# Kernel tuning notes

Measured on AMD Instinct MI355X. Metric: run time of the kernel, lower is better.

## Reference

```python
import jax, jax.numpy as jnp
import numpy as np

HID, E, S, L_CAP, EPS = 768, 1536, 128, 512, 1e-5


def _rope_seq(x):
    """RoPE along axis 1. x: [b, n, 2, s]."""
    n, s = x.shape[1], x.shape[-1]
    half = s // 2
    inv_freq = jnp.power(10000.0, -jnp.arange(half, dtype=x.dtype) / half)  # [half]
    sinusoid = jnp.arange(n, dtype=x.dtype)[:, None, None] * inv_freq       # [n,1,half]
    sin, cos = jnp.sin(sinusoid), jnp.cos(sinusoid)
    x1, x2 = jnp.split(x, 2, axis=-1)
    return jnp.concatenate([x1 * cos - x2 * sin, x2 * cos + x1 * sin], axis=-1)


def setup_inputs() -> dict:
    key = jax.random.key(0)
    ks = jax.random.split(key, 6)
    B, L = 32, 512
    return {
        "x": jax.random.normal(ks[0], (B, L, HID), dtype=jnp.float32),
        "ln_gamma": jnp.ones((HID,), jnp.float32),
        "ln_beta": jnp.zeros((HID,), jnp.float32),
        "uv_W": jax.random.normal(ks[1], (HID, 2 * E + S), jnp.float32) * 0.02,
        "uv_b": jnp.zeros((2 * E + S,), jnp.float32),
        "gamma_qk": jax.random.normal(ks[2], (2, S), jnp.float32) * 0.02,
        "beta_qk": jnp.zeros((2, S), jnp.float32),
        "w_rel": jax.random.normal(ks[3], (2 * L_CAP - 1,), jnp.float32) * 0.02,
        "o_W": jax.random.normal(ks[4], (E, HID), jnp.float32) * 0.02,
        "o_b": jnp.zeros((HID,), jnp.float32),
    }


def reference(x, ln_gamma, ln_beta, uv_W, uv_b, gamma_qk, beta_qk, w_rel, o_W, o_b):
    L = x.shape[1]
    shortcut = x
    # LayerNorm
    mu = jnp.mean(x, axis=-1, keepdims=True)
    var = jnp.mean(jnp.square(x - mu), axis=-1, keepdims=True)
    xn = (x - mu) * jax.lax.rsqrt(var + EPS) * ln_gamma + ln_beta
    # uv projection + silu, split into u, v, base
    uv = jax.nn.silu(xn @ uv_W + uv_b)                       # [b, n, 2e+s]
    u, v, base = jnp.split(uv, [E, 2 * E], axis=-1)          # [b,n,e], [b,n,e], [b,n,s]
    # per-head affine then RoPE -> q, k
    base = base[..., None, :] * gamma_qk + beta_qk           # [b, n, 2, s]
    base = _rope_seq(base)
    q, k = base[..., 0, :], base[..., 1, :]
    # relu^2 attention kernel with Toeplitz relative position bias
    qk = jnp.einsum('bnd,bmd->bnm', q, k)
    idx = jnp.arange(L)
    bias = w_rel[idx[None, :] - idx[:, None] + L - 1]        # bias[i,j] = w[j-i+L-1]
    kernel = jnp.square(jax.nn.relu(qk / L + bias))
    # gated value aggregation + output projection + residual
    out = u * jnp.einsum('bnm,bme->bne', kernel, v)
    out = out @ o_W + o_b
    return out + shortcut
```

## Files before the change

### kernel.cpp

```cpp
#include <hip/hip_runtime.h>
#include <hip/hip_bf16.h>
#include <math.h>

typedef __bf16 bf16x8 __attribute__((ext_vector_type(8)));
typedef float f32x4 __attribute__((ext_vector_type(4)));
typedef unsigned short u16x4 __attribute__((ext_vector_type(4)));

#define AS1P const __attribute__((address_space(1))) void*
#define AS3P __attribute__((address_space(3))) void*

__device__ __forceinline__ float b2f(unsigned short h) {
    unsigned int u = ((unsigned int)h) << 16;
    return __builtin_bit_cast(float, u);
}
__device__ __forceinline__ unsigned short f2b(float f) {
    unsigned int u = __builtin_bit_cast(unsigned int, f);
    u += 0x7FFFu + ((u >> 16) & 1u);
    return (unsigned short)(u >> 16);
}
__device__ __forceinline__ float silu(float c) {
    return c * __builtin_amdgcn_rcpf(1.0f + __expf(-c));
}

__global__ __launch_bounds__(256) void k_convT(const float* __restrict__ src,
                                               unsigned short* __restrict__ dst,
                                               int R, int C) {
    __shared__ float tile[32][33];
    int tx = threadIdx.x, ty = threadIdx.y;
    int r0 = blockIdx.y << 5, c0 = blockIdx.x << 5;
#pragma unroll
    for (int i = 0; i < 4; ++i)
        tile[ty + 8 * i][tx] = src[(long long)(r0 + ty + 8 * i) * C + c0 + tx];
    __syncthreads();
#pragma unroll
    for (int i = 0; i < 4; ++i)
        dst[(long long)(c0 + ty + 8 * i) * R + r0 + tx] = f2b(tile[tx][ty + 8 * i]);
}

__global__ __launch_bounds__(256) void k_ln(const float* __restrict__ x,
                                            const float* __restrict__ g,
                                            const float* __restrict__ b,
                                            unsigned short* __restrict__ xn) {
    int row = blockIdx.x;
    int t = threadIdx.x;
    const float* xr = x + (long long)row * 768;
    float v0 = xr[t], v1 = xr[t + 256], v2 = xr[t + 512];
    float s = v0 + v1 + v2;
    float q = v0 * v0 + v1 * v1 + v2 * v2;
#pragma unroll
    for (int off = 32; off > 0; off >>= 1) {
        s += __shfl_xor(s, off);
        q += __shfl_xor(q, off);
    }
    __shared__ float ss[4], sq[4];
    int w = t >> 6;
    if ((t & 63) == 0) { ss[w] = s; sq[w] = q; }
    __syncthreads();
    float S_ = ss[0] + ss[1] + ss[2] + ss[3];
    float Q_ = sq[0] + sq[1] + sq[2] + sq[3];
    float mu = S_ * (1.0f / 768.0f);
    float var = Q_ * (1.0f / 768.0f) - mu * mu;
    float rs = rsqrtf(var + 1e-5f);
    unsigned short* xo = xn + (long long)row * 768;
    xo[t]       = f2b((v0 - mu) * rs * g[t]       + b[t]);
    xo[t + 256] = f2b((v1 - mu) * rs * g[t + 256] + b[t + 256]);
    xo[t + 512] = f2b((v2 - mu) * rs * g[t + 512] + b[t + 512]);
}

__global__ __launch_bounds__(128) void k_rope(const unsigned short* __restrict__ bS,
                                              const float* __restrict__ gqk,
                                              const float* __restrict__ bqk,
                                              unsigned short* __restrict__ q,
                                              unsigned short* __restrict__ k) {
    int row = blockIdx.x;
    int l = row & 511;
    int s = threadIdx.x;
    int j = s & 63;
    int partner = s ^ 64;
    float b0 = b2f(bS[(long long)row * 128 + s]);
    float bp = b2f(bS[(long long)row * 128 + partner]);
    float invf = __expf((float)j * -0.14391156831f);
    float th = (float)l * invf;
    float sn, cs;
    __sincosf(th, &sn, &cs);
    float sign = (s < 64) ? -1.0f : 1.0f;
    float preq  = b0 * gqk[s]           + bqk[s];
    float preqp = bp * gqk[partner]     + bqk[partner];
    q[(long long)row * 128 + s] = f2b(preq * cs + sign * preqp * sn);
    float prek  = b0 * gqk[128 + s]       + bqk[128 + s];
    float prekp = bp * gqk[128 + partner] + bqk[128 + partner];
    k[(long long)row * 128 + s] = f2b(prek * cs + sign * prekp * sn);
}

__global__ __launch_bounds__(256) void k_qk(const unsigned short* __restrict__ A,
                                            const unsigned short* __restrict__ B,
                                            const float* __restrict__ wrel,
                                            unsigned short* __restrict__ P) {
    __shared__ __align__(16) unsigned short As[128 * 64];
    __shared__ __align__(16) unsigned short Bs[128 * 64];
    int t = threadIdx.x;
    int w = t >> 6, lane = t & 63;
    int wr = w >> 1, wc = w & 1;
    int bx = blockIdx.x, by = blockIdx.y, bz = blockIdx.z;
    {
        int gx = gridDim.x, gy = gridDim.y;
        int nb = gx * gy * gridDim.z;
        int bid = (bz * gy + by) * gx + bx;
        int s = (bid & 7) * (nb >> 3) + (bid >> 3);
        bx = s % gx;
        by = (s / gx) % gy;
        bz = s / (gx * gy);
    }
    const unsigned short* Ab = A + (long long)bz * 512 * 128 + (long long)by * 128 * 128;
    const unsigned short* Bb = B + (long long)bz * 512 * 128 + (long long)bx * 128 * 128;

    f32x4 acc[4][4];
#pragma unroll
    for (int m = 0; m < 4; ++m)
#pragma unroll
        for (int n = 0; n < 4; ++n) acc[m][n] = (f32x4){0.f, 0.f, 0.f, 0.f};

    int rowA = (w << 3) + (lane >> 3);
    int colA = (lane & 7) << 3;

    for (int k0 = 0; k0 < 128; k0 += 64) {
#pragma unroll
        for (int i = 0; i < 4; ++i) {
            int r = (i << 5) + rowA;
            __builtin_amdgcn_global_load_lds(
                (AS1P)(Ab + (long long)r * 128 + k0 + colA),
                (AS3P)(&As[(i << 11) + (w << 9)]), 16, 0, 0);
            __builtin_amdgcn_global_load_lds(
                (AS1P)(Bb + (long long)r * 128 + k0 + colA),
                (AS3P)(&Bs[(i << 11) + (w << 9)]), 16, 0, 0);
        }
        __syncthreads();
#pragma unroll
        for (int ks = 0; ks < 2; ++ks) {
            bf16x8 af[4], bfr[4];
#pragma unroll
            for (int m = 0; m < 4; ++m)
                af[m] = *(const bf16x8*)&As[((wr << 6) + (m << 4) + (lane & 15)) * 64 +
                                            (ks << 5) + ((lane >> 4) << 3)];
#pragma unroll
            for (int n = 0; n < 4; ++n)
                bfr[n] = *(const bf16x8*)&Bs[((wc << 6) + (n << 4) + (lane & 15)) * 64 +
                                             (ks << 5) + ((lane >> 4) << 3)];
#pragma unroll
            for (int m = 0; m < 4; ++m)
#pragma unroll
                for (int n = 0; n < 4; ++n)
                    acc[m][n] = __builtin_amdgcn_mfma_f32_16x16x32_bf16(bfr[n], af[m],
                                                                        acc[m][n], 0, 0, 0);
        }
        __syncthreads();
    }

    int c15 = lane & 15, qq = lane >> 4;
    int rowb = (by << 7) + (wr << 6) + c15;
    int colb = (bx << 7) + (wc << 6) + (qq << 2);
#pragma unroll
    for (int m = 0; m < 4; ++m) {
#pragma unroll
        for (int n = 0; n < 4; ++n) {
            int grow = rowb + (m << 4);
            int gcol = colb + (n << 4);
            f32x4 a = acc[m][n];
            int base = gcol - grow + 511;
            u16x4 o;
#pragma unroll
            for (int i = 0; i < 4; ++i) {
                float val = a[i] * (1.0f / 512.0f) + wrel[base + i];
                val = fmaxf(val, 0.0f);
                o[i] = f2b(val * val);
            }
            *(u16x4*)(P + ((long long)(bz * 512 + grow)) * 512 + gcol) = o;
        }
    }
}

__device__ __forceinline__ bf16x8 ldsread(const unsigned short* p) {
    bf16x8 r;
    unsigned int off =
        (unsigned int)(unsigned long long)(__attribute__((address_space(3))) const void*)p;
    asm volatile("ds_read_b128 %0, %1" : "=v"(r) : "v"(off));
    return r;
}
__device__ __forceinline__ void stage_half(const unsigned short* __restrict__ g, int ldk,
                                           unsigned short* lds, int t) {
#pragma unroll
    for (int i = 0; i < 2; ++i) {
        int slot = t + (i << 9);
        int row = slot >> 2;
        int gs = (slot & 3) ^ ((slot >> 3) & 3);
        __builtin_amdgcn_global_load_lds(
            (AS1P)(g + (long long)row * ldk + (gs << 3)),
            (AS3P)(lds + slot * 8), 16, 0, 0);
    }
}

template <bool SWAP, int NT>
__device__ __forceinline__ void kloop8(const unsigned short* __restrict__ Ab,
                                       const unsigned short* __restrict__ Bb,
                                       unsigned short* As, unsigned short* Bs,
                                       f32x4 (&acc)[8][4], int tid,
                                       int wr, int wc, int c15, int qq, int gq) {
    constexpr int K = NT * 64;
    stage_half(Ab, K, As + 0, tid);
    stage_half(Bb, K, Bs + 0, tid);
    stage_half(Ab + 32, K, As + 8192, tid);
    stage_half(Bb + 32, K, Bs + 8192, tid);
    stage_half(Ab + 64, K, As + 16384, tid);
    stage_half(Bb + 64, K, Bs + 16384, tid);
    asm volatile("s_waitcnt vmcnt(8)" ::: "memory");
    __builtin_amdgcn_s_barrier();

    bf16x8 bfr[4], af[4];
    for (int t = 0; t < NT; ++t) {
        const int b = t & 1;
        const unsigned short* A0 = As + b * 16384;
        const unsigned short* B0 = Bs + b * 16384;
#pragma unroll
        for (int p = 0; p < 4; ++p) {
            const int ks = p >> 1, mh = p & 1;
            const unsigned short* At = A0 + ks * 8192;
            const unsigned short* Bt = B0 + ks * 8192;
            if (mh == 0) {
#pragma unroll
                for (int n = 0; n < 4; ++n)
                    bfr[n] = ldsread(Bt + (wc * 64 + n * 16 + c15) * 32 + gq * 8);
            }
#pragma unroll
            for (int j = 0; j < 4; ++j)
                af[j] = ldsread(At + (wr * 128 + (mh * 4 + j) * 16 + c15) * 32 + gq * 8);
            if (p == 0) {
                if (t + 1 < NT)
                    stage_half(Ab + (t + 1) * 64 + 32, K,
                               As + (((t + 1) & 1) * 2 + 1) * 8192, tid);
            } else if (p == 1) {
                if (t + 1 < NT)
                    stage_half(Bb + (t + 1) * 64 + 32, K,
                               Bs + (((t + 1) & 1) * 2 + 1) * 8192, tid);
            } else if (p == 2) {
                if (t + 2 < NT)
                    stage_half(Ab + (t + 2) * 64, K, As + (b * 2) * 8192, tid);
            } else {
                if (t + 2 < NT)
                    stage_half(Bb + (t + 2) * 64, K, Bs + (b * 2) * 8192, tid);
            }
            __builtin_amdgcn_s_barrier();
            asm volatile("s_waitcnt lgkmcnt(0)" ::: "memory");
            __builtin_amdgcn_sched_barrier(0);
            __builtin_amdgcn_s_setprio(1);
#pragma unroll
            for (int j = 0; j < 4; ++j)
#pragma unroll
                for (int n = 0; n < 4; ++n) {
                    if constexpr (SWAP)
                        acc[mh * 4 + j][n] = __builtin_amdgcn_mfma_f32_16x16x32_bf16(
                            bfr[n], af[j], acc[mh * 4 + j][n], 0, 0, 0);
                    else
                        acc[mh * 4 + j][n] = __builtin_amdgcn_mfma_f32_16x16x32_bf16(
                            af[j], bfr[n], acc[mh * 4 + j][n], 0, 0, 0);
                }
            __builtin_amdgcn_s_setprio(0);
            if (p == 1) {
                if (t < NT - 1)
                    asm volatile("s_waitcnt vmcnt(8)" ::: "memory");
                else
                    asm volatile("s_waitcnt vmcnt(0)" ::: "memory");
            } else if (p == 3) {
                if (t < NT - 2)
                    asm volatile("s_waitcnt vmcnt(8)" ::: "memory");
                else if (t == NT - 2)
                    asm volatile("s_waitcnt vmcnt(4)" ::: "memory");
            }
            __builtin_amdgcn_sched_barrier(0);
            __builtin_amdgcn_s_barrier();
        }
    }
}

template <int EPI, int SWZ, int NT>
__global__ __launch_bounds__(512, 2) void k8(const unsigned short* __restrict__ A,
                                             const unsigned short* __restrict__ B,
                                             long long strideA, long long strideB,
                                             void* p0, void* p1, void* p2,
                                             const void* p3) {
    constexpr int K = NT * 64;
    __shared__ __align__(16) unsigned short As[2][2][256 * 32];
    __shared__ __align__(16) unsigned short Bs[2][2][256 * 32];
    int tid = threadIdx.x;
    int w = tid >> 6, lane = tid & 63;
    int wr = w >> 2, wc = w & 3;
    int c15 = lane & 15, qq = lane >> 4;
    int gq = qq ^ ((c15 >> 1) & 3);
    int bx = blockIdx.x, by = blockIdx.y, bz = blockIdx.z;
    if constexpr (SWZ == 1) {
        int gx = gridDim.x;
        int nb = gx * gridDim.y;
        int bid = by * gx + bx;
        int s = (bid & 7) * (nb >> 3) + (bid >> 3);
        bx = s % gx;
        by = s / gx;
    } else if constexpr (SWZ == 2) {
        int gx = gridDim.x, gy = gridDim.y;
        int nb = gx * gy * gridDim.z;
        int bid = (bz * gy + by) * gx + bx;
        int s = (bid & 7) * (nb >> 3) + (bid >> 3);
        bx = s % gx;
        by = (s / gx) % gy;
        bz = s / (gx * gy);
    }
    const unsigned short* Ab = A + bz * strideA + (long long)by * 256 * K;
    const unsigned short* Bb = B + bz * strideB + (long long)bx * 256 * K;

    f32x4 acc[8][4];
#pragma unroll
    for (int m = 0; m < 8; ++m)
#pragma unroll
        for (int n = 0; n < 4; ++n) acc[m][n] = (f32x4){0.f, 0.f, 0.f, 0.f};

    bool swapped = true;
    if constexpr (EPI == 10) {
        swapped = !(bx >= 6 && bx < 12);
        if (swapped)
            kloop8<true, NT>(Ab, Bb, &As[0][0][0], &Bs[0][0][0], acc, tid, wr, wc, c15, qq, gq);
        else
            kloop8<false, NT>(Ab, Bb, &As[0][0][0], &Bs[0][0][0], acc, tid, wr, wc, c15, qq, gq);
    } else {
        kloop8<true, NT>(Ab, Bb, &As[0][0][0], &Bs[0][0][0], acc, tid, wr, wc, c15, qq, gq);
    }

    if constexpr (EPI == 10) {
        if (swapped) {
            int rowb = by * 256 + wr * 128 + c15;
            int colb = bx * 256 + wc * 64 + (qq << 2);
#pragma unroll
            for (int m = 0; m < 8; ++m) {
#pragma unroll
                for (int n = 0; n < 4; ++n) {
                    int R = rowb + m * 16;
                    int C = colb + n * 16;
                    f32x4 a = acc[m][n];
                    if (C < 1536) {
                        f32x4 bb = *(const f32x4*)((const float*)p3 + C);
                        u16x4 o;
#pragma unroll
                        for (int i = 0; i < 4; ++i) o[i] = f2b(silu(a[i] + bb[i]));
                        *(u16x4*)((unsigned short*)p0 + (long long)R * 1536 + C) = o;
                    } else if (C < 3200) {
                        f32x4 bb = *(const f32x4*)((const float*)p3 + C);
                        u16x4 o;
#pragma unroll
                        for (int i = 0; i < 4; ++i) o[i] = f2b(silu(a[i] + bb[i]));
                        *(u16x4*)((unsigned short*)p2 + (long long)R * 128 + (C - 3072)) = o;
                    }
                }
            }
        } else {
            int rowb = by * 256 + wr * 128 + (qq << 2);
            int colb = bx * 256 + wc * 64 + c15;
#pragma unroll
            for (int m = 0; m < 8; ++m) {
#pragma unroll
                for (int n = 0; n < 4; ++n) {
                    int R = rowb + m * 16;
                    int C = colb + n * 16;
                    float bias = ((const float*)p3)[C];
                    f32x4 a = acc[m][n];
                    u16x4 o;
#pragma unroll
                    for (int i = 0; i < 4; ++i) o[i] = f2b(silu(a[i] + bias));
                    int bb2 = R >> 9, mm = R & 511;
                    *(u16x4*)((unsigned short*)p1 +
                              ((long long)bb2 * 1536 + (C - 1536)) * 512 + mm) = o;
                }
            }
        }
    } else if constexpr (EPI == 2) {
        int rowb = by * 256 + wr * 128 + c15;
        int colb = bx * 256 + wc * 64 + (qq << 2);
#pragma unroll
        for (int m = 0; m < 8; ++m) {
#pragma unroll
            for (int n = 0; n < 4; ++n) {
                int R = rowb + m * 16;
                int C = colb + n * 16;
                f32x4 a = acc[m][n];
                long long idx = ((long long)(bz * 512 + R)) * 1536 + C;
                u16x4 uu = *(const u16x4*)((const unsigned short*)p1 + idx);
                u16x4 o;
#pragma unroll
                for (int i = 0; i < 4; ++i) o[i] = f2b(a[i] * b2f(uu[i]));
                *(u16x4*)((unsigned short*)p0 + idx) = o;
            }
        }
    } else {
        int rowb = by * 256 + wr * 128 + c15;
        int colb = bx * 256 + wc * 64 + (qq << 2);
#pragma unroll
        for (int m = 0; m < 8; ++m) {
#pragma unroll
            for (int n = 0; n < 4; ++n) {
                int R = rowb + m * 16;
                int C = colb + n * 16;
                f32x4 a = acc[m][n];
                long long idx = (long long)R * 768 + C;
                f32x4 xv = *(const f32x4*)((const float*)p2 + idx);
                f32x4 ob = *(const f32x4*)((const float*)p1 + C);
                f32x4 o;
#pragma unroll
                for (int i = 0; i < 4; ++i) o[i] = a[i] + ob[i] + xv[i];
                *(f32x4*)((float*)p0 + idx) = o;
            }
        }
    }
}

extern "C" void kernel_launch(void* const* d_in, const int* in_sizes, int n_in,
                              void* d_out, int out_size, void* d_ws, size_t ws_size,
                              hipStream_t stream) {
    const float* x     = (const float*)d_in[0];
    const float* ln_g  = (const float*)d_in[1];
    const float* ln_b  = (const float*)d_in[2];
    const float* uv_W  = (const float*)d_in[3];
    const float* uv_b  = (const float*)d_in[4];
    const float* g_qk  = (const float*)d_in[5];
    const float* b_qk  = (const float*)d_in[6];
    const float* w_rel = (const float*)d_in[7];
    const float* o_W   = (const float*)d_in[8];
    const float* o_b   = (const float*)d_in[9];
    float* out = (float*)d_out;

    char* ws = (char*)d_ws;
    size_t off = 0;
    auto alloc = [&](size_t bytes) {
        void* p = ws + off;
        off += (bytes + 255) & ~(size_t)255;
        return p;
    };
    unsigned short* uvWT = (unsigned short*)alloc(3328ll * 768 * 2);
    unsigned short* oWT  = (unsigned short*)alloc(768ll * 1536 * 2);
    unsigned short* xn   = (unsigned short*)alloc(16384ll * 768 * 2);
    unsigned short* u    = (unsigned short*)alloc(16384ll * 1536 * 2);
    unsigned short* vT   = (unsigned short*)alloc(32ll * 1536 * 512 * 2);
    unsigned short* bS   = (unsigned short*)alloc(16384ll * 128 * 2);
    unsigned short* q    = (unsigned short*)alloc(32ll * 512 * 128 * 2);
    unsigned short* k    = (unsigned short*)alloc(32ll * 512 * 128 * 2);
    unsigned short* P     = xn;
    unsigned short* gated = u;

    k_convT<<<dim3(100, 24), dim3(32, 8), 0, stream>>>(uv_W, uvWT, 768, 3200);
    k_convT<<<dim3(24, 48), dim3(32, 8), 0, stream>>>(o_W, oWT, 1536, 768);
    k_ln<<<16384, 256, 0, stream>>>(x, ln_g, ln_b, xn);
    k8<10, 1, 12><<<dim3(13, 64), 512, 0, stream>>>(
        xn, uvWT, 0, 0, (void*)u, (void*)vT, (void*)bS, (const void*)uv_b);
    k_rope<<<16384, 128, 0, stream>>>(bS, g_qk, b_qk, q, k);
    k_qk<<<dim3(4, 4, 32), 256, 0, stream>>>(q, k, w_rel, P);
    k8<2, 2, 8><<<dim3(6, 2, 32), 512, 0, stream>>>(
        P, vT, 512ll * 512, 1536ll * 512, (void*)gated, (void*)u, nullptr, nullptr);
    k8<3, 1, 24><<<dim3(3, 64), 512, 0, stream>>>(
        gated, oWT, 0, 0, (void*)out, (void*)o_b, (void*)x, nullptr);
}
```

Baseline: 284.0 us.

## Restructure GEMM k-loop to one-stage-ahead prefetch with compiler-scheduled LDS reads

Rewrites the main 256x256 GEMM k-loop so it prefetches only the next k-tile into the other LDS buffer, instead of keeping tiles two steps ahead. The inline-asm ds_read_b128 helper and the per-phase lgkmcnt waits are replaced by plain vector loads through macros, which leaves the compiler to schedule the LDS reads. Barriers are rearranged around the four MFMA phases per tile. This cuts in-flight global loads and explicit waits, but it risks exposing more global-load latency because prefetch depth is shallower.

```diff
diff --git a/kernel.cpp b/kernel.cpp
--- a/kernel.cpp
+++ b/kernel.cpp
@@ -179,13 +179,6 @@
     }
 }
 
-__device__ __forceinline__ bf16x8 ldsread(const unsigned short* p) {
-    bf16x8 r;
-    unsigned int off =
-        (unsigned int)(unsigned long long)(__attribute__((address_space(3))) const void*)p;
-    asm volatile("ds_read_b128 %0, %1" : "=v"(r) : "v"(off));
-    return r;
-}
 __device__ __forceinline__ void stage_half(const unsigned short* __restrict__ g, int ldk,
                                            unsigned short* lds, int t) {
 #pragma unroll
@@ -199,86 +192,85 @@
     }
 }
 
+#define BARF() { __builtin_amdgcn_s_barrier(); asm volatile("" ::: "memory"); }
+
 template <bool SWAP, int NT>
 __device__ __forceinline__ void kloop8(const unsigned short* __restrict__ Ab,
                                        const unsigned short* __restrict__ Bb,
                                        unsigned short* As, unsigned short* Bs,
                                        f32x4 (&acc)[8][4], int tid,
-                                       int wr, int wc, int c15, int qq, int gq) {
+                                       int wr, int wc, int c15, int gq) {
     constexpr int K = NT * 64;
     stage_half(Ab, K, As + 0, tid);
     stage_half(Bb, K, Bs + 0, tid);
     stage_half(Ab + 32, K, As + 8192, tid);
     stage_half(Bb + 32, K, Bs + 8192, tid);
-    stage_half(Ab + 64, K, As + 16384, tid);
-    stage_half(Bb + 64, K, Bs + 16384, tid);
-    asm volatile("s_waitcnt vmcnt(8)" ::: "memory");
-    __builtin_amdgcn_s_barrier();
-
-    bf16x8 bfr[4], af[4];
+    asm volatile("s_waitcnt vmcnt(4)" ::: "memory");
+    BARF()
+
+#define LOADB(KS)                                                              \
+    _Pragma("unroll") for (int n = 0; n < 4; ++n)                              \
+        bfr[n] = *(const bf16x8*)(B0 + (KS) * 8192 +                           \
+                     ((wc << 6) + (n << 4) + c15) * 32 + (gq << 3));
+#define LOADA(KS, MH)                                                          \
+    _Pragma("unroll") for (int j = 0; j < 4; ++j)                              \
+        af[j] = *(const bf16x8*)(A0 + (KS) * 8192 +                            \
+                     ((wr << 7) + ((MH) << 6) + (j << 4) + c15) * 32 + (gq << 3));
+#define DO16(MH)                                                               \
+    __builtin_amdgcn_s_setprio(1);                                             \
+    _Pragma("unroll") for (int j = 0; j < 4; ++j)                              \
+        _Pragma("unroll") for (int n = 0; n < 4; ++n) {                        \
+            if constexpr (SWAP)                                                \
+                acc[(MH) * 4 + j][n] = __builtin_amdgcn_mfma_f32_16x16x32_bf16(\
+                    bfr[n], af[j], acc[(MH) * 4 + j][n], 0, 0, 0);             \
+            else                                                               \
+                acc[(MH) * 4 + j][n] = __builtin_amdgcn_mfma_f32_16x16x32_bf16(\
+                    af[j], bfr[n], acc[(MH) * 4 + j][n], 0, 0, 0);             \
+        }                                                                      \
+    __builtin_amdgcn_s_setprio(0);
+
     for (int t = 0; t < NT; ++t) {
         const int b = t & 1;
         const unsigned short* A0 = As + b * 16384;
         const unsigned short* B0 = Bs + b * 16384;
-#pragma unroll
-        for (int p = 0; p < 4; ++p) {
-            const int ks = p >> 1, mh = p & 1;
-            const unsigned short* At = A0 + ks * 8192;
-            const unsigned short* Bt = B0 + ks * 8192;
-            if (mh == 0) {
-#pragma unroll
-                for (int n = 0; n < 4; ++n)
-                    bfr[n] = ldsread(Bt + (wc * 64 + n * 16 + c15) * 32 + gq * 8);
-            }
-#pragma unroll
-            for (int j = 0; j < 4; ++j)
-                af[j] = ldsread(At + (wr * 128 + (mh * 4 + j) * 16 + c15) * 32 + gq * 8);
-            if (p == 0) {
-                if (t + 1 < NT)
-                    stage_half(Ab + (t + 1) * 64 + 32, K,
-                               As + (((t + 1) & 1) * 2 + 1) * 8192, tid);
-            } else if (p == 1) {
-                if (t + 1 < NT)
-                    stage_half(Bb + (t + 1) * 64 + 32, K,
-                               Bs + (((t + 1) & 1) * 2 + 1) * 8192, tid);
-            } else if (p == 2) {
-                if (t + 2 < NT)
-                    stage_half(Ab + (t + 2) * 64, K, As + (b * 2) * 8192, tid);
-            } else {
-                if (t + 2 < NT)
-                    stage_half(Bb + (t + 2) * 64, K, Bs + (b * 2) * 8192, tid);
-            }
-            __builtin_amdgcn_s_barrier();
-            asm volatile("s_waitcnt lgkmcnt(0)" ::: "memory");
-            __builtin_amdgcn_sched_barrier(0);
-            __builtin_amdgcn_s_setprio(1);
-#pragma unroll
-            for (int j = 0; j < 4; ++j)
-#pragma unroll
-                for (int n = 0; n < 4; ++n) {
-                    if constexpr (SWAP)
-                        acc[mh * 4 + j][n] = __builtin_amdgcn_mfma_f32_16x16x32_bf16(
-                            bfr[n], af[j], acc[mh * 4 + j][n], 0, 0, 0);
-                    else
-                        acc[mh * 4 + j][n] = __builtin_amdgcn_mfma_f32_16x16x32_bf16(
-                            af[j], bfr[n], acc[mh * 4 + j][n], 0, 0, 0);
-                }
-            __builtin_amdgcn_s_setprio(0);
-            if (p == 1) {
-                if (t < NT - 1)
-                    asm volatile("s_waitcnt vmcnt(8)" ::: "memory");
-                else
-                    asm volatile("s_waitcnt vmcnt(0)" ::: "memory");
-            } else if (p == 3) {
-                if (t < NT - 2)
-                    asm volatile("s_waitcnt vmcnt(8)" ::: "memory");
-                else if (t == NT - 2)
-                    asm volatile("s_waitcnt vmcnt(4)" ::: "memory");
-            }
-            __builtin_amdgcn_sched_barrier(0);
-            __builtin_amdgcn_s_barrier();
-        }
-    }
+        unsigned short* An = As + (b ^ 1) * 16384;
+        unsigned short* Bn = Bs + (b ^ 1) * 16384;
+        const unsigned short* Ag = Ab + (t + 1) * 64;
+        const unsigned short* Bg = Bb + (t + 1) * 64;
+        const bool pf = (t + 1 < NT);
+        bf16x8 bfr[4], af[4];
+        LOADB(0)
+        LOADA(0, 0)
+        if (pf) stage_half(Ag, K, An, tid);
+        BARF()
+        DO16(0)
+        BARF()
+        LOADA(0, 1)
+        if (pf) stage_half(Bg, K, Bn, tid);
+        BARF()
+        DO16(1)
+        if (t < NT - 1)
+            asm volatile("s_waitcnt vmcnt(4)" ::: "memory");
+        else
+            asm volatile("s_waitcnt vmcnt(0)" ::: "memory");
+        BARF()
+        LOADB(1)
+        LOADA(1, 0)
+        if (pf) stage_half(Ag + 32, K, An + 8192, tid);
+        BARF()
+        DO16(0)
+        BARF()
+        LOADA(1, 1)
+        if (pf) stage_half(Bg + 32, K, Bn + 8192, tid);
+        BARF()
+        DO16(1)
+        if (t < NT - 1)
+            asm volatile("s_waitcnt vmcnt(4)" ::: "memory");
+        BARF()
+    }
+#undef LOADB
+#undef LOADA
+#undef DO16
 }
 
 template <int EPI, int SWZ, int NT>
@@ -325,11 +317,11 @@
     if constexpr (EPI == 10) {
         swapped = !(bx >= 6 && bx < 12);
         if (swapped)
-            kloop8<true, NT>(Ab, Bb, &As[0][0][0], &Bs[0][0][0], acc, tid, wr, wc, c15, qq, gq);
+            kloop8<true, NT>(Ab, Bb, &As[0][0][0], &Bs[0][0][0], acc, tid, wr, wc, c15, gq);
         else
-            kloop8<false, NT>(Ab, Bb, &As[0][0][0], &Bs[0][0][0], acc, tid, wr, wc, c15, qq, gq);
+            kloop8<false, NT>(Ab, Bb, &As[0][0][0], &Bs[0][0][0], acc, tid, wr, wc, c15, gq);
     } else {
-        kloop8<true, NT>(Ab, Bb, &As[0][0][0], &Bs[0][0][0], acc, tid, wr, wc, c15, qq, gq);
+        kloop8<true, NT>(Ab, Bb, &As[0][0][0], &Bs[0][0][0], acc, tid, wr, wc, c15, gq);
     }
 
     if constexpr (EPI == 10) {
```

Result: slower. 319.0 us (+12.3%).
